# Optimization experiments

Measured on AMD Instinct MI355X. Metric: run time of the kernel, lower is better.

Reference implementation:

```python
import jax, jax.numpy as jnp
import numpy as np

B, S, IN, OUT = 4, 4096, 4096, 4096

def setup_inputs() -> dict:
    key = jax.random.key(0)
    k1, k2, k3 = jax.random.split(key, 3)
    x = jax.random.normal(k1, (B, S, IN), dtype=jnp.float32)
    # packed ternary weight: (sign+1) in {0,1,2}, stored as small int
    packed_w = jax.random.randint(k2, (OUT, IN), 0, 3, dtype=jnp.int32)
    # alpha = mean(|W|) surrogate; act_scale = max|x|/127 surrogate
    alpha = jnp.float32(0.02)
    act_scale = jnp.float32(4.0 / 127.0)
    bias = jax.random.normal(k3, (OUT,), dtype=jnp.float32)
    return {"x": x, "packed_w": packed_w, "alpha": alpha, "act_scale": act_scale, "bias": bias}

def reference(x, packed_w, alpha, act_scale, bias):
    # Activation fake-quant (int8 symmetric): round(x/scale), clamp, dequant.
    # torch uses act_scale.item() -> scale is a constant w.r.t. autodiff.
    scale = jax.lax.stop_gradient(jnp.maximum(act_scale, 1e-5))
    x_int = jnp.clip(jnp.round(x / scale), -127.0, 127.0)
    x_dq = jnp.nan_to_num(x_int * scale, nan=0.0, posinf=10000.0, neginf=-10000.0)
    # Ternary weight dequant: (packed - 1) * alpha, values in {-a, 0, +a}
    w = (packed_w.astype(jnp.float32) - 1.0) * alpha  # [OUT, IN]
    # F.linear: x @ W^T + b
    return jnp.einsum('bsi,oi->bso', x_dq, w) + bias
```

## Files before the change

### kernel.cpp

```cpp
#include <hip/hip_runtime.h>
#include <hip/hip_bf16.h>

typedef int v4i __attribute__((ext_vector_type(4)));

#define M_DIM 16384
#define N_DIM 4096
#define K_DIM 4096
#define BM 256
#define BN 256
#define BKB 128
#define NT (K_DIM / BKB)

#define QBLK 2048
#define PBLK 512

__global__ void prep_kernel(const float4* __restrict__ x, int4* __restrict__ qx, int n16x,
                            const int4* __restrict__ w, int4* __restrict__ qw, int n16w,
                            const float* __restrict__ act_scale) {
  if (blockIdx.x < QBLK) {
    const float s = fmaxf(act_scale[0], 1e-5f);
    const float inv_s = 1.0f / s;
#define PKQ(v) (( (int)fminf(fmaxf(rintf((v).x * inv_s), -127.f), 127.f) & 0xff)        | \
               (((int)fminf(fmaxf(rintf((v).y * inv_s), -127.f), 127.f) & 0xff) << 8)  | \
               (((int)fminf(fmaxf(rintf((v).z * inv_s), -127.f), 127.f) & 0xff) << 16) | \
               (((int)fminf(fmaxf(rintf((v).w * inv_s), -127.f), 127.f) & 0xff) << 24))
    int i = blockIdx.x * blockDim.x + threadIdx.x;
    const int stride = QBLK * blockDim.x;
    for (; i < n16x; i += stride) {
      const float4* xp = x + (size_t)i * 4;
      float4 v0 = xp[0], v1 = xp[1], v2 = xp[2], v3 = xp[3];
      int4 o;
      o.x = PKQ(v0); o.y = PKQ(v1); o.z = PKQ(v2); o.w = PKQ(v3);
      qx[i] = o;
    }
  } else {
#define PKW(v) ((((v).x - 1) & 0xff) | ((((v).y - 1) & 0xff) << 8) | \
                ((((v).z - 1) & 0xff) << 16) | ((((v).w - 1) & 0xff) << 24))
    int i = (blockIdx.x - QBLK) * blockDim.x + threadIdx.x;
    const int stride = PBLK * blockDim.x;
    for (; i < n16w; i += stride) {
      const int4* wp = w + (size_t)i * 4;
      int4 v0 = wp[0], v1 = wp[1], v2 = wp[2], v3 = wp[3];
      int4 o;
      o.x = PKW(v0); o.y = PKW(v1); o.z = PKW(v2); o.w = PKW(v3);
      qw[i] = o;
    }
  }
}

__global__ __launch_bounds__(512, 2) void bitlinear_gemm(
    const signed char* __restrict__ A,
    const signed char* __restrict__ B,
    const float* __restrict__ bias,
    const float* __restrict__ alpha_p,
    const float* __restrict__ act_scale_p,
    float* __restrict__ out) {
  __shared__ __align__(16) signed char As[2][BM * BKB];
  __shared__ __align__(16) signed char Bs[2][BN * BKB];

  const int t = threadIdx.x;
  const int lane = t & 63, wid = t >> 6;
  const int wm = wid >> 2, wn = wid & 3;
  const int l15 = lane & 15, l4 = lane >> 4;

  const int nwg = (M_DIM / BM) * (N_DIM / BN);
  const int wg = (blockIdx.x & 7) * (nwg >> 3) + (blockIdx.x >> 3);
  const int bm = wg / (N_DIM / BN);
  const int bn = wg % (N_DIM / BN);

  const signed char* aGl = A + ((size_t)(bm * BM + (t >> 3))) * K_DIM + (t & 7) * 16;
  const signed char* bGl = B + ((size_t)(bn * BN + (t >> 3))) * K_DIM + (t & 7) * 16;
  const int wrOff = (t >> 3) * 128 + (((t & 7) ^ ((t >> 3) & 7)) * 16);

  v4i sA[4], sB[4];

#define GL_A(u, P) sA[u] = *(const v4i*)((P) + (size_t)((u) * 64) * K_DIM)
#define GL_B(u, P) sB[u] = *(const v4i*)((P) + (size_t)((u) * 64) * K_DIM)
#define WR_A(BUF) { _Pragma("unroll") for (int u = 0; u < 4; ++u) \
    *(v4i*)&As[BUF][u * 8192 + wrOff] = sA[u]; }
#define WR_B(BUF) { _Pragma("unroll") for (int u = 0; u < 4; ++u) \
    *(v4i*)&Bs[BUF][u * 8192 + wrOff] = sB[u]; }

  const int l7 = l15 & 7;
  const int soK0 = ((0 + l4) ^ l7) * 16;
  const int soK1 = ((4 + l4) ^ l7) * 16;
  const int aRd = (wm * 128 + l15) * BKB;
  const int bRd = (wn * 64 + l15) * BKB;

  v4i acc[8][4] = {};
  v4i bF[4][2], aF[2][2];

#define LOAD_B(buf) \
  { _Pragma("unroll") for (int nc = 0; nc < 4; ++nc) { \
      bF[nc][0] = *(const v4i*)&Bs[buf][bRd + nc * 2048 + soK0]; \
      bF[nc][1] = *(const v4i*)&Bs[buf][bRd + nc * 2048 + soK1]; } }

#define LOAD_A(buf, q) \
  aF[0][0] = *(const v4i*)&As[buf][aRd + (2*(q)) * 2048 + soK0]; \
  aF[0][1] = *(const v4i*)&As[buf][aRd + (2*(q)) * 2048 + soK1]; \
  aF[1][0] = *(const v4i*)&As[buf][aRd + (2*(q)+1) * 2048 + soK0]; \
  aF[1][1] = *(const v4i*)&As[buf][aRd + (2*(q)+1) * 2048 + soK1];

#define MFMA_Q(q) \
  { _Pragma("unroll") for (int nc = 0; nc < 4; ++nc) { \
      acc[2*(q)][nc]   = __builtin_amdgcn_mfma_i32_16x16x64_i8(aF[0][0], bF[nc][0], acc[2*(q)][nc], 0, 0, 0); \
      acc[2*(q)][nc]   = __builtin_amdgcn_mfma_i32_16x16x64_i8(aF[0][1], bF[nc][1], acc[2*(q)][nc], 0, 0, 0); \
      acc[2*(q)+1][nc] = __builtin_amdgcn_mfma_i32_16x16x64_i8(aF[1][0], bF[nc][0], acc[2*(q)+1][nc], 0, 0, 0); \
      acc[2*(q)+1][nc] = __builtin_amdgcn_mfma_i32_16x16x64_i8(aF[1][1], bF[nc][1], acc[2*(q)+1][nc], 0, 0, 0); } }

#define BAR __builtin_amdgcn_s_barrier()

#define TILE_BODY(BUF, PA, PB) do { \
    LOAD_B(BUF); LOAD_A(BUF, 0); \
    GL_B(0, PB); GL_B(1, PB); \
    __builtin_amdgcn_s_setprio(1); MFMA_Q(0); __builtin_amdgcn_s_setprio(0); \
    LOAD_A(BUF, 1); \
    GL_B(2, PB); GL_B(3, PB); \
    __builtin_amdgcn_s_setprio(1); MFMA_Q(1); __builtin_amdgcn_s_setprio(0); \
    LOAD_A(BUF, 2); \
    GL_A(0, PA); GL_A(1, PA); GL_A(2, PA); GL_A(3, PA); \
    __builtin_amdgcn_s_setprio(1); MFMA_Q(2); __builtin_amdgcn_s_setprio(0); \
    WR_B(BUF^1); \
    LOAD_A(BUF, 3); \
    __builtin_amdgcn_s_setprio(1); MFMA_Q(3); __builtin_amdgcn_s_setprio(0); \
    WR_A(BUF^1); \
    asm volatile("s_waitcnt lgkmcnt(0)" ::: "memory"); \
    BAR; \
  } while (0)

#define TILE_LAST(BUF) do { \
    LOAD_B(BUF); LOAD_A(BUF, 0); \
    __builtin_amdgcn_s_setprio(1); MFMA_Q(0); __builtin_amdgcn_s_setprio(0); \
    LOAD_A(BUF, 1); \
    __builtin_amdgcn_s_setprio(1); MFMA_Q(1); __builtin_amdgcn_s_setprio(0); \
    LOAD_A(BUF, 2); \
    __builtin_amdgcn_s_setprio(1); MFMA_Q(2); __builtin_amdgcn_s_setprio(0); \
    LOAD_A(BUF, 3); \
    __builtin_amdgcn_s_setprio(1); MFMA_Q(3); __builtin_amdgcn_s_setprio(0); \
  } while (0)

  GL_B(0, bGl); GL_B(1, bGl); GL_B(2, bGl); GL_B(3, bGl);
  GL_A(0, aGl); GL_A(1, aGl); GL_A(2, aGl); GL_A(3, aGl);
  asm volatile("s_waitcnt vmcnt(0)" ::: "memory");
  WR_B(0); WR_A(0);
  asm volatile("s_waitcnt lgkmcnt(0)" ::: "memory");
  BAR;
  __builtin_amdgcn_sched_barrier(0);

  const signed char* aGk = aGl;
  const signed char* bGk = bGl;
  for (int it = 0; it < NT / 2 - 1; ++it) {
    TILE_BODY(0, aGk + BKB,     bGk + BKB);
    TILE_BODY(1, aGk + 2 * BKB, bGk + 2 * BKB);
    aGk += 2 * BKB; bGk += 2 * BKB;
  }
  TILE_BODY(0, aGk + BKB, bGk + BKB);
  TILE_LAST(1);

  const float sA_ = fmaxf(act_scale_p[0], 1e-5f) * alpha_p[0];
  const int gn0 = bn * BN + wn * 64 + l15;
  const int gm0 = bm * BM + wm * 128 + l4 * 4;
#pragma unroll
  for (int nc = 0; nc < 4; ++nc) {
    const float bv = bias[gn0 + nc * 16];
#pragma unroll
    for (int mr = 0; mr < 8; ++mr) {
#pragma unroll
      for (int r = 0; r < 4; ++r) {
        const int gm = gm0 + mr * 16 + r;
        out[(size_t)gm * N_DIM + gn0 + nc * 16] = (float)acc[mr][nc][r] * sA_ + bv;
      }
    }
  }
}

extern "C" void kernel_launch(void* const* d_in, const int* in_sizes, int n_in,
                              void* d_out, int out_size, void* d_ws, size_t ws_size,
                              hipStream_t stream) {
  const float* x      = (const float*)d_in[0];
  const int*   pw     = (const int*)d_in[1];
  const float* alpha  = (const float*)d_in[2];
  const float* act_sc = (const float*)d_in[3];
  const float* bias   = (const float*)d_in[4];
  float* out = (float*)d_out;

  signed char* x8 = (signed char*)d_ws;
  signed char* w8 = (signed char*)d_ws + (size_t)M_DIM * K_DIM;

  prep_kernel<<<QBLK + PBLK, 256, 0, stream>>>(
      (const float4*)x, (int4*)x8, M_DIM * K_DIM / 16,
      (const int4*)pw, (int4*)w8, N_DIM * K_DIM / 16, act_sc);

  dim3 grid((M_DIM / BM) * (N_DIM / BN));
  bitlinear_gemm<<<grid, 512, 0, stream>>>(x8, w8, bias, alpha, act_sc, out);
}
```

Before: 362.7 us.

## Split GEMM tile across 16 waves with 1024-thread blocks

Raises the GEMM block from 512 to 1024 threads, so each of 16 waves computes a 64x64 sub-tile instead of 128x64, halving per-thread accumulators and global-load staging. The global-to-LDS copy mapping is reworked so each thread loads two 16-byte chunks from one row instead of four rows. The aim is more waves per CU to hide latency and lower register pressure. The cost is one block per CU, and the same LDS bytes are now shared by more waves, with more barrier participants and fewer MFMAs per LDS read.

```diff
diff --git a/kernel.cpp b/kernel.cpp
--- a/kernel.cpp
+++ b/kernel.cpp
@@ -48,7 +48,7 @@
   }
 }
 
-__global__ __launch_bounds__(512, 2) void bitlinear_gemm(
+__global__ __launch_bounds__(1024, 1) void bitlinear_gemm(
     const signed char* __restrict__ A,
     const signed char* __restrict__ B,
     const float* __restrict__ bias,
@@ -68,61 +68,56 @@
   const int bm = wg / (N_DIM / BN);
   const int bn = wg % (N_DIM / BN);
 
-  const signed char* aGl = A + ((size_t)(bm * BM + (t >> 3))) * K_DIM + (t & 7) * 16;
-  const signed char* bGl = B + ((size_t)(bn * BN + (t >> 3))) * K_DIM + (t & 7) * 16;
-  const int wrOff = (t >> 3) * 128 + (((t & 7) ^ ((t >> 3) & 7)) * 16);
+  const signed char* aGl = A + ((size_t)(bm * BM + (t >> 2))) * K_DIM + (t & 3) * 16;
+  const signed char* bGl = B + ((size_t)(bn * BN + (t >> 2))) * K_DIM + (t & 3) * 16;
+  const int wr0 = (t >> 2) * 128 + ((((t & 3) + 0) ^ ((t >> 2) & 7)) * 16);
+  const int wr1 = (t >> 2) * 128 + ((((t & 3) + 4) ^ ((t >> 2) & 7)) * 16);
 
-  v4i sA[4], sB[4];
+  v4i sA[2], sB[2];
 
-#define GL_A(u, P) sA[u] = *(const v4i*)((P) + (size_t)((u) * 64) * K_DIM)
-#define GL_B(u, P) sB[u] = *(const v4i*)((P) + (size_t)((u) * 64) * K_DIM)
-#define WR_A(BUF) { _Pragma("unroll") for (int u = 0; u < 4; ++u) \
-    *(v4i*)&As[BUF][u * 8192 + wrOff] = sA[u]; }
-#define WR_B(BUF) { _Pragma("unroll") for (int u = 0; u < 4; ++u) \
-    *(v4i*)&Bs[BUF][u * 8192 + wrOff] = sB[u]; }
+#define GL_A(u, P) sA[u] = *(const v4i*)((P) + (u) * 64)
+#define GL_B(u, P) sB[u] = *(const v4i*)((P) + (u) * 64)
+#define WR_A(BUF) { *(v4i*)&As[BUF][wr0] = sA[0]; *(v4i*)&As[BUF][wr1] = sA[1]; }
+#define WR_B(BUF) { *(v4i*)&Bs[BUF][wr0] = sB[0]; *(v4i*)&Bs[BUF][wr1] = sB[1]; }
 
   const int l7 = l15 & 7;
   const int soK0 = ((0 + l4) ^ l7) * 16;
   const int soK1 = ((4 + l4) ^ l7) * 16;
-  const int aRd = (wm * 128 + l15) * BKB;
+  const int aRd = (wm * 64 + l15) * BKB;
   const int bRd = (wn * 64 + l15) * BKB;
 
-  v4i acc[8][4] = {};
-  v4i bF[4][2], aF[2][2];
+  v4i acc[4][4] = {};
+  v4i bF[4][2], aF[2];
 
 #define LOAD_B(buf) \
   { _Pragma("unroll") for (int nc = 0; nc < 4; ++nc) { \
       bF[nc][0] = *(const v4i*)&Bs[buf][bRd + nc * 2048 + soK0]; \
       bF[nc][1] = *(const v4i*)&Bs[buf][bRd + nc * 2048 + soK1]; } }
 
-#define LOAD_A(buf, q) \
-  aF[0][0] = *(const v4i*)&As[buf][aRd + (2*(q)) * 2048 + soK0]; \
-  aF[0][1] = *(const v4i*)&As[buf][aRd + (2*(q)) * 2048 + soK1]; \
-  aF[1][0] = *(const v4i*)&As[buf][aRd + (2*(q)+1) * 2048 + soK0]; \
-  aF[1][1] = *(const v4i*)&As[buf][aRd + (2*(q)+1) * 2048 + soK1];
+#define LOAD_A(buf, m) \
+  aF[0] = *(const v4i*)&As[buf][aRd + (m) * 2048 + soK0]; \
+  aF[1] = *(const v4i*)&As[buf][aRd + (m) * 2048 + soK1];
 
-#define MFMA_Q(q) \
+#define MFMA_M(m) \
   { _Pragma("unroll") for (int nc = 0; nc < 4; ++nc) { \
-      acc[2*(q)][nc]   = __builtin_amdgcn_mfma_i32_16x16x64_i8(aF[0][0], bF[nc][0], acc[2*(q)][nc], 0, 0, 0); \
-      acc[2*(q)][nc]   = __builtin_amdgcn_mfma_i32_16x16x64_i8(aF[0][1], bF[nc][1], acc[2*(q)][nc], 0, 0, 0); \
-      acc[2*(q)+1][nc] = __builtin_amdgcn_mfma_i32_16x16x64_i8(aF[1][0], bF[nc][0], acc[2*(q)+1][nc], 0, 0, 0); \
-      acc[2*(q)+1][nc] = __builtin_amdgcn_mfma_i32_16x16x64_i8(aF[1][1], bF[nc][1], acc[2*(q)+1][nc], 0, 0, 0); } }
+      acc[m][nc] = __builtin_amdgcn_mfma_i32_16x16x64_i8(aF[0], bF[nc][0], acc[m][nc], 0, 0, 0); \
+      acc[m][nc] = __builtin_amdgcn_mfma_i32_16x16x64_i8(aF[1], bF[nc][1], acc[m][nc], 0, 0, 0); } }
 
 #define BAR __builtin_amdgcn_s_barrier()
 
 #define TILE_BODY(BUF, PA, PB) do { \
     LOAD_B(BUF); LOAD_A(BUF, 0); \
-    GL_B(0, PB); GL_B(1, PB); \
-    __builtin_amdgcn_s_setprio(1); MFMA_Q(0); __builtin_amdgcn_s_setprio(0); \
+    GL_B(0, PB); \
+    __builtin_amdgcn_s_setprio(1); MFMA_M(0); __builtin_amdgcn_s_setprio(0); \
     LOAD_A(BUF, 1); \
-    GL_B(2, PB); GL_B(3, PB); \
-    __builtin_amdgcn_s_setprio(1); MFMA_Q(1); __builtin_amdgcn_s_setprio(0); \
+    GL_B(1, PB); \
+    __builtin_amdgcn_s_setprio(1); MFMA_M(1); __builtin_amdgcn_s_setprio(0); \
     LOAD_A(BUF, 2); \
-    GL_A(0, PA); GL_A(1, PA); GL_A(2, PA); GL_A(3, PA); \
-    __builtin_amdgcn_s_setprio(1); MFMA_Q(2); __builtin_amdgcn_s_setprio(0); \
+    GL_A(0, PA); GL_A(1, PA); \
+    __builtin_amdgcn_s_setprio(1); MFMA_M(2); __builtin_amdgcn_s_setprio(0); \
     WR_B(BUF^1); \
     LOAD_A(BUF, 3); \
-    __builtin_amdgcn_s_setprio(1); MFMA_Q(3); __builtin_amdgcn_s_setprio(0); \
+    __builtin_amdgcn_s_setprio(1); MFMA_M(3); __builtin_amdgcn_s_setprio(0); \
     WR_A(BUF^1); \
     asm volatile("s_waitcnt lgkmcnt(0)" ::: "memory"); \
     BAR; \
@@ -130,17 +125,17 @@
 
 #define TILE_LAST(BUF) do { \
     LOAD_B(BUF); LOAD_A(BUF, 0); \
-    __builtin_amdgcn_s_setprio(1); MFMA_Q(0); __builtin_amdgcn_s_setprio(0); \
+    __builtin_amdgcn_s_setprio(1); MFMA_M(0); __builtin_amdgcn_s_setprio(0); \
     LOAD_A(BUF, 1); \
-    __builtin_amdgcn_s_setprio(1); MFMA_Q(1); __builtin_amdgcn_s_setprio(0); \
+    __builtin_amdgcn_s_setprio(1); MFMA_M(1); __builtin_amdgcn_s_setprio(0); \
     LOAD_A(BUF, 2); \
-    __builtin_amdgcn_s_setprio(1); MFMA_Q(2); __builtin_amdgcn_s_setprio(0); \
+    __builtin_amdgcn_s_setprio(1); MFMA_M(2); __builtin_amdgcn_s_setprio(0); \
     LOAD_A(BUF, 3); \
-    __builtin_amdgcn_s_setprio(1); MFMA_Q(3); __builtin_amdgcn_s_setprio(0); \
+    __builtin_amdgcn_s_setprio(1); MFMA_M(3); __builtin_amdgcn_s_setprio(0); \
   } while (0)
 
-  GL_B(0, bGl); GL_B(1, bGl); GL_B(2, bGl); GL_B(3, bGl);
-  GL_A(0, aGl); GL_A(1, aGl); GL_A(2, aGl); GL_A(3, aGl);
+  GL_B(0, bGl); GL_B(1, bGl);
+  GL_A(0, aGl); GL_A(1, aGl);
   asm volatile("s_waitcnt vmcnt(0)" ::: "memory");
   WR_B(0); WR_A(0);
   asm volatile("s_waitcnt lgkmcnt(0)" ::: "memory");
@@ -159,12 +154,12 @@
 
   const float sA_ = fmaxf(act_scale_p[0], 1e-5f) * alpha_p[0];
   const int gn0 = bn * BN + wn * 64 + l15;
-  const int gm0 = bm * BM + wm * 128 + l4 * 4;
+  const int gm0 = bm * BM + wm * 64 + l4 * 4;
 #pragma unroll
   for (int nc = 0; nc < 4; ++nc) {
     const float bv = bias[gn0 + nc * 16];
 #pragma unroll
-    for (int mr = 0; mr < 8; ++mr) {
+    for (int mr = 0; mr < 4; ++mr) {
 #pragma unroll
       for (int r = 0; r < 4; ++r) {
         const int gm = gm0 + mr * 16 + r;
@@ -192,5 +187,5 @@
       (const int4*)pw, (int4*)w8, N_DIM * K_DIM / 16, act_sc);
 
   dim3 grid((M_DIM / BM) * (N_DIM / BN));
-  bitlinear_gemm<<<grid, 512, 0, stream>>>(x8, w8, bias, alpha, act_sc, out);
+  bitlinear_gemm<<<grid, 1024, 0, stream>>>(x8, w8, bias, alpha, act_sc, out);
 }
```

Measured after the change: 538.4 us. 48.5% more time.
